# Optimization experiments

Measured on AMD Instinct MI355X. Metric: run time of the kernel, lower is better.

The kernel has to match this reference:

```python
import jax, jax.numpy as jnp
import numpy as np

DIM = 128
N_NODES = 100000
N_EDGES = 1600000


def setup_inputs() -> dict:
    key = jax.random.key(0)
    ks = jax.random.split(key, 9)
    x1 = jax.random.normal(ks[0], (N_NODES, DIM), dtype=jnp.float32)
    x2 = jax.random.normal(ks[1], (N_NODES, DIM), dtype=jnp.float32)
    edge_index = jax.random.randint(ks[2], (2, N_EDGES), 0, N_NODES, dtype=jnp.int64)
    # make_mlp(2*dim, dim, 1, layers=3): Linear(256,128)+ReLU, Linear(128,128)+ReLU, Linear(128,1)
    def lin(k, fan_in, fan_out):
        bound = 1.0 / np.sqrt(fan_in)
        kw, kb = jax.random.split(k)
        W = jax.random.uniform(kw, (fan_in, fan_out), jnp.float32, -bound, bound)
        b = jax.random.uniform(kb, (fan_out,), jnp.float32, -bound, bound)
        return W, b
    W1, b1 = lin(ks[3], 2 * DIM, DIM)
    W2, b2 = lin(ks[4], DIM, DIM)
    W3, b3 = lin(ks[5], DIM, 1)
    return {"x1": x1, "x2": x2, "edge_index": edge_index,
            "W1": W1, "b1": b1, "W2": W2, "b2": b2, "W3": W3, "b3": b3}


def reference(x1, x2, edge_index, W1, b1, W2, b2, W3, b3):
    # Gather endpoints per edge: [E, dim] each
    xs = x1[edge_index[0]]
    xt = x2[edge_index[1]]
    pair = jnp.concatenate([xs, xt], axis=-1)  # [E, 2*dim]
    h = jax.nn.relu(pair @ W1 + b1)            # [E, dim]
    h = jax.nn.relu(h @ W2 + b2)               # [E, dim]
    return h @ W3 + b3                         # [E, 1]
```

## Files before the change

### kernel.cpp

```cpp
#include <hip/hip_runtime.h>
#include <cstdint>

#define DIM 128
#define MTILE 64
#define PAIR_LD 264
#define H_LD 136

typedef __bf16 v8bf __attribute__((ext_vector_type(8)));
typedef float v16f __attribute__((ext_vector_type(16)));

static __device__ __forceinline__ unsigned int f2bf_pack(float a, float b) {
  union { float f; unsigned u; } x, y; x.f = a; y.f = b;
  unsigned lo = (x.u + 0x7FFFu + ((x.u >> 16) & 1u)) >> 16;
  unsigned hi = (y.u + 0x7FFFu + ((y.u >> 16) & 1u)) >> 16;
  return lo | (hi << 16);
}
static __device__ __forceinline__ unsigned short f2bf(float a) {
  union { float f; unsigned u; } x; x.f = a;
  return (unsigned short)((x.u + 0x7FFFu + ((x.u >> 16) & 1u)) >> 16);
}
static __device__ __forceinline__ float bfhi2f(unsigned int hi16) {
  union { unsigned u; float f; } c; c.u = hi16; return c.f;
}

__global__ __launch_bounds__(256) void prep_all(
    const float* __restrict__ W1, const float* __restrict__ W2,
    const float* __restrict__ x1, const float* __restrict__ x2,
    unsigned short* __restrict__ W1t, unsigned short* __restrict__ W2t,
    unsigned short* __restrict__ xc1, unsigned short* __restrict__ xc2,
    int n8, int use_cache) {
  int i = blockIdx.x * 256 + threadIdx.x;
  if (i < 32768) {
    int n = i >> 8, k = i & 255;
    W1t[i] = f2bf(W1[k * 128 + n]);
  } else if (i < 49152) {
    int j = i - 32768;
    int n = j >> 7, k = j & 127;
    W2t[j] = f2bf(W2[k * 128 + n]);
  } else if (use_cache) {
    int j = i - 49152;
    const float* xs;
    unsigned short* xd;
    if (j < n8) { xs = x1; xd = xc1; }
    else if (j < 2 * n8) { xs = x2; xd = xc2; j -= n8; }
    else return;
    const float4* s = reinterpret_cast<const float4*>(xs) + (size_t)j * 2;
    float4 f0 = s[0];
    float4 f1 = s[1];
    uint4 pk;
    pk.x = f2bf_pack(f0.x, f0.y);
    pk.y = f2bf_pack(f0.z, f0.w);
    pk.z = f2bf_pack(f1.x, f1.y);
    pk.w = f2bf_pack(f1.z, f1.w);
    reinterpret_cast<uint4*>(xd)[j] = pk;
  }
}

__global__ __launch_bounds__(256, 2) void mlp_edge_cached(
    const int* __restrict__ eidx,
    const unsigned short* __restrict__ W1t, const unsigned short* __restrict__ W2t,
    const float* __restrict__ b1, const float* __restrict__ b2,
    const float* __restrict__ W3, const float* __restrict__ b3,
    float* __restrict__ out, int E, int ntiles,
    const unsigned short* __restrict__ xc1, const unsigned short* __restrict__ xc2)
{
  __shared__ unsigned short sm_pair[MTILE * PAIR_LD];
  __shared__ unsigned short sm_h1[MTILE * H_LD];
  __shared__ float sm_part[4 * MTILE];

  const int tid = threadIdx.x;
  const int lane = tid & 63;
  const int wv = tid >> 6;
  const int l31 = lane & 31;
  const int l5 = lane >> 5;
  const int nb = wv * 32 + l31;

  v8bf B1[16], B2[8];
#pragma unroll
  for (int kt = 0; kt < 16; ++kt)
    B1[kt] = *reinterpret_cast<const v8bf*>(W1t + nb * 256 + kt * 16 + l5 * 8);
#pragma unroll
  for (int kt = 0; kt < 8; ++kt)
    B2[kt] = *reinterpret_cast<const v8bf*>(W2t + nb * 128 + kt * 16 + l5 * 8);
  const float b1v = b1[nb];
  const float bias3 = b3[0];

  float w3r[16], b2r[16];
#pragma unroll
  for (int r = 0; r < 16; ++r) {
    int n2 = wv * 32 + (r & 3) + 8 * (r >> 2) + 4 * l5;
    w3r[r] = W3[n2];
    b2r[r] = b2[n2];
  }

  const int rslot = tid >> 4;
  const int lane16 = tid & 15;

  int idxr[8];
  {
    const int t0 = min((int)blockIdx.x, ntiles - 1);
    const size_t e0 = (size_t)t0 * MTILE;
#pragma unroll
    for (int p = 0; p < 8; ++p) {
      int el = (p & 3) * 16 + rslot;
      idxr[p] = eidx[e0 + el + ((p >= 4) ? (size_t)E : 0)];
    }
  }

  int eprev = -1;

  for (int tile = blockIdx.x; tile < ntiles; tile += gridDim.x) {
    __syncthreads();

    uint4 xv[8];
#pragma unroll
    for (int p = 0; p < 8; ++p) {
      const unsigned short* xb = (p >= 4) ? xc2 : xc1;
      xv[p] = *reinterpret_cast<const uint4*>(xb + (size_t)idxr[p] * DIM + lane16 * 8);
    }

    if (eprev >= 0 && tid < MTILE) {
      float s = sm_part[tid] + sm_part[64 + tid] + sm_part[128 + tid] + sm_part[192 + tid];
      out[eprev + tid] = s + bias3;
    }

#pragma unroll
    for (int p = 0; p < 8; ++p) {
      int el = (p & 3) * 16 + rslot;
      *reinterpret_cast<uint4*>(&sm_pair[el * PAIR_LD + ((p >= 4) ? 128 : 0) + lane16 * 8]) = xv[p];
    }

    {
      const int tn = min(tile + (int)gridDim.x, ntiles - 1);
      const size_t en = (size_t)tn * MTILE;
#pragma unroll
      for (int p = 0; p < 8; ++p) {
        int el = (p & 3) * 16 + rslot;
        idxr[p] = eidx[en + el + ((p >= 4) ? (size_t)E : 0)];
      }
    }
    __syncthreads();

#pragma unroll
    for (int h = 0; h < 2; ++h) {
      v16f acc;
#pragma unroll
      for (int r = 0; r < 16; ++r) acc[r] = 0.f;
#pragma unroll
      for (int kt = 0; kt < 16; ++kt) {
        v8bf a = *reinterpret_cast<const v8bf*>(&sm_pair[(32 * h + l31) * PAIR_LD + kt * 16 + l5 * 8]);
        acc = __builtin_amdgcn_mfma_f32_32x32x16_bf16(a, B1[kt], acc, 0, 0, 0);
      }
#pragma unroll
      for (int r = 0; r < 16; ++r) {
        int m = 32 * h + (r & 3) + 8 * (r >> 2) + 4 * l5;
        sm_h1[m * H_LD + nb] = f2bf(fmaxf(acc[r] + b1v, 0.f));
      }
    }
    __syncthreads();

#pragma unroll
    for (int h = 0; h < 2; ++h) {
      v16f acc;
#pragma unroll
      for (int r = 0; r < 16; ++r) acc[r] = b2r[r];
#pragma unroll
      for (int kt = 0; kt < 8; ++kt) {
        v8bf bf = *reinterpret_cast<const v8bf*>(&sm_h1[(32 * h + l31) * H_LD + kt * 16 + l5 * 8]);
        acc = __builtin_amdgcn_mfma_f32_32x32x16_bf16(B2[kt], bf, acc, 0, 0, 0);
      }
      float p = 0.f;
#pragma unroll
      for (int r = 0; r < 16; ++r) p += fmaxf(acc[r], 0.f) * w3r[r];
      p += __shfl_xor(p, 32);
      if (l5 == 0) sm_part[wv * 64 + 32 * h + l31] = p;
    }

    eprev = tile * MTILE;
  }

  __syncthreads();
  if (eprev >= 0 && tid < MTILE) {
    float s = sm_part[tid] + sm_part[64 + tid] + sm_part[128 + tid] + sm_part[192 + tid];
    out[eprev + tid] = s + bias3;
  }
}

__global__ __launch_bounds__(256, 2) void mlp_edge_direct(
    const float* __restrict__ x1, const float* __restrict__ x2,
    const int* __restrict__ eidx,
    const unsigned short* __restrict__ W1t, const unsigned short* __restrict__ W2t,
    const float* __restrict__ b1, const float* __restrict__ b2,
    const float* __restrict__ W3, const float* __restrict__ b3,
    float* __restrict__ out, int E, int ntiles)
{
  __shared__ unsigned short sm_pair[MTILE * PAIR_LD];
  __shared__ unsigned short sm_h1[MTILE * H_LD];
  __shared__ float sm_w3[4 * 36];
  unsigned short* sm_h2 = sm_pair;

  const int tid = threadIdx.x;
  const int lane = tid & 63;
  const int wv = tid >> 6;
  const int l31 = lane & 31;
  const int l5 = lane >> 5;
  const int nb = wv * 32 + l31;

  v8bf B1[16], B2[8];
#pragma unroll
  for (int kt = 0; kt < 16; ++kt)
    B1[kt] = *reinterpret_cast<const v8bf*>(W1t + nb * 256 + kt * 16 + l5 * 8);
#pragma unroll
  for (int kt = 0; kt < 8; ++kt)
    B2[kt] = *reinterpret_cast<const v8bf*>(W2t + nb * 128 + kt * 16 + l5 * 8);
  const float b1v = b1[nb];
  const float b2v = b2[nb];
  const float bias3 = b3[0];
  if (tid < 128) sm_w3[(tid >> 5) * 36 + (tid & 31)] = W3[tid];

  const int rslot = tid >> 4;
  const int lane16 = tid & 15;
  const int part = tid & 3;

  for (int tile = blockIdx.x; tile < ntiles; tile += gridDim.x) {
    __syncthreads();
    const int e0 = tile * MTILE;
#pragma unroll
    for (int p = 0; p < 8; ++p) {
      int rowid = p * 16 + rslot;
      int half = rowid >> 6;
      int el = rowid & 63;
      int node = eidx[e0 + el + (half ? E : 0)];
      const float* src = (half ? x2 : x1) + (size_t)node * DIM + lane16 * 8;
      float4 f0 = *reinterpret_cast<const float4*>(src);
      float4 f1 = *reinterpret_cast<const float4*>(src + 4);
      uint4 pk;
      pk.x = f2bf_pack(f0.x, f0.y);
      pk.y = f2bf_pack(f0.z, f0.w);
      pk.z = f2bf_pack(f1.x, f1.y);
      pk.w = f2bf_pack(f1.z, f1.w);
      *reinterpret_cast<uint4*>(&sm_pair[el * PAIR_LD + half * 128 + lane16 * 8]) = pk;
    }
    __syncthreads();

    v16f acc0, acc1;
#pragma unroll
    for (int r = 0; r < 16; ++r) { acc0[r] = 0.f; acc1[r] = 0.f; }
#pragma unroll
    for (int kt = 0; kt < 16; ++kt) {
      v8bf a0 = *reinterpret_cast<const v8bf*>(&sm_pair[l31 * PAIR_LD + kt * 16 + l5 * 8]);
      v8bf a1 = *reinterpret_cast<const v8bf*>(&sm_pair[(32 + l31) * PAIR_LD + kt * 16 + l5 * 8]);
      acc0 = __builtin_amdgcn_mfma_f32_32x32x16_bf16(a0, B1[kt], acc0, 0, 0, 0);
      acc1 = __builtin_amdgcn_mfma_f32_32x32x16_bf16(a1, B1[kt], acc1, 0, 0, 0);
    }
#pragma unroll
    for (int r = 0; r < 16; ++r) {
      int m = (r & 3) + 8 * (r >> 2) + 4 * l5;
      sm_h1[m * H_LD + nb] = f2bf(fmaxf(acc0[r] + b1v, 0.f));
      sm_h1[(32 + m) * H_LD + nb] = f2bf(fmaxf(acc1[r] + b1v, 0.f));
    }
    __syncthreads();

    v16f c0, c1;
#pragma unroll
    for (int r = 0; r < 16; ++r) { c0[r] = 0.f; c1[r] = 0.f; }
#pragma unroll
    for (int kt = 0; kt < 8; ++kt) {
      v8bf a0 = *reinterpret_cast<const v8bf*>(&sm_h1[l31 * H_LD + kt * 16 + l5 * 8]);
      v8bf a1 = *reinterpret_cast<const v8bf*>(&sm_h1[(32 + l31) * H_LD + kt * 16 + l5 * 8]);
      c0 = __builtin_amdgcn_mfma_f32_32x32x16_bf16(a0, B2[kt], c0, 0, 0, 0);
      c1 = __builtin_amdgcn_mfma_f32_32x32x16_bf16(a1, B2[kt], c1, 0, 0, 0);
    }
#pragma unroll
    for (int r = 0; r < 16; ++r) {
      int m = (r & 3) + 8 * (r >> 2) + 4 * l5;
      sm_h2[m * H_LD + nb] = f2bf(fmaxf(c0[r] + b2v, 0.f));
      sm_h2[(32 + m) * H_LD + nb] = f2bf(fmaxf(c1[r] + b2v, 0.f));
    }
    __syncthreads();

    {
      int el = tid >> 2;
      const unsigned short* hrow = &sm_h2[el * H_LD + part * 32];
      const float* wrow = &sm_w3[part * 36];
      float sum = 0.f;
#pragma unroll
      for (int j = 0; j < 4; ++j) {
        uint4 u = *reinterpret_cast<const uint4*>(hrow + j * 8);
        float4 wa = *reinterpret_cast<const float4*>(wrow + j * 8);
        float4 wb = *reinterpret_cast<const float4*>(wrow + j * 8 + 4);
        sum += bfhi2f(u.x << 16) * wa.x + bfhi2f(u.x & 0xFFFF0000u) * wa.y;
        sum += bfhi2f(u.y << 16) * wa.z + bfhi2f(u.y & 0xFFFF0000u) * wa.w;
        sum += bfhi2f(u.z << 16) * wb.x + bfhi2f(u.z & 0xFFFF0000u) * wb.y;
        sum += bfhi2f(u.w << 16) * wb.z + bfhi2f(u.w & 0xFFFF0000u) * wb.w;
      }
      sum += __shfl_xor(sum, 1, 64);
      sum += __shfl_xor(sum, 2, 64);
      if (part == 0) out[e0 + el] = sum + bias3;
    }
  }
}

extern "C" void kernel_launch(void* const* d_in, const int* in_sizes, int n_in,
                              void* d_out, int out_size, void* d_ws, size_t ws_size,
                              hipStream_t stream) {
  const float* x1 = (const float*)d_in[0];
  const float* x2 = (const float*)d_in[1];
  const int* eidx = (const int*)d_in[2];
  const float* W1 = (const float*)d_in[3];
  const float* b1 = (const float*)d_in[4];
  const float* W2 = (const float*)d_in[5];
  const float* b2 = (const float*)d_in[6];
  const float* W3 = (const float*)d_in[7];
  const float* b3 = (const float*)d_in[8];
  float* out = (float*)d_out;

  int E = in_sizes[2] / 2;
  if (E <= 0) return;
  int ntiles = E / MTILE;
  int nelem = in_sizes[0];
  int n8 = nelem / 8;

  unsigned short* W1t = (unsigned short*)d_ws;
  unsigned short* W2t = W1t + 32768;
  size_t woff = 98304;
  size_t need = woff + 2 * (size_t)nelem * 2;
  int use_cache = (ws_size >= need) ? 1 : 0;
  unsigned short* xc1 = (unsigned short*)((char*)d_ws + woff);
  unsigned short* xc2 = xc1 + nelem;

  int prep_items = 49152 + (use_cache ? 2 * n8 : 0);
  prep_all<<<(prep_items + 255) / 256, 256, 0, stream>>>(
      W1, W2, x1, x2, W1t, W2t, xc1, xc2, n8, use_cache);

  if (use_cache) {
    mlp_edge_cached<<<512, 256, 0, stream>>>(eidx, W1t, W2t, b1, b2, W3, b3,
                                             out, E, ntiles, xc1, xc2);
  } else {
    mlp_edge_direct<<<512, 256, 0, stream>>>(x1, x2, eidx, W1t, W2t,
                                             b1, b2, W3, b3, out, E, ntiles);
  }
}
```

Baseline: 315.6 us.

## Precompute first-layer projections per node and gather projected features per edge

Because the first linear layer is linear in the concatenated inputs, x1@W1a and x2@W1b+b1 are computed once per node in a new kernel and stored as fp16. The edge kernel then gathers the two projected rows, adds them, applies ReLU and runs only the second GEMM, using fp16 MFMA. This cuts first-layer MFMA work from per edge (1.6M) to per node (200k) and drops the pair shared-memory buffer, which allows higher occupancy and a larger grid. The cost is an extra launch and fp16 rounding of the layer-one outputs, which differs slightly from bf16 numerics.

```diff
diff --git a/kernel.cpp b/kernel.cpp
--- a/kernel.cpp
+++ b/kernel.cpp
@@ -7,6 +7,7 @@
 #define H_LD 136
 
 typedef __bf16 v8bf __attribute__((ext_vector_type(8)));
+typedef _Float16 v8hf __attribute__((ext_vector_type(8)));
 typedef float v16f __attribute__((ext_vector_type(16)));
 
 static __device__ __forceinline__ unsigned int f2bf_pack(float a, float b) {
@@ -19,16 +20,17 @@
   union { float f; unsigned u; } x; x.f = a;
   return (unsigned short)((x.u + 0x7FFFu + ((x.u >> 16) & 1u)) >> 16);
 }
+static __device__ __forceinline__ unsigned short f2h(float a) {
+  union { _Float16 h; unsigned short u; } c; c.h = (_Float16)a; return c.u;
+}
 static __device__ __forceinline__ float bfhi2f(unsigned int hi16) {
   union { unsigned u; float f; } c; c.u = hi16; return c.f;
 }
 
-__global__ __launch_bounds__(256) void prep_all(
+__global__ __launch_bounds__(256) void prep_w(
     const float* __restrict__ W1, const float* __restrict__ W2,
-    const float* __restrict__ x1, const float* __restrict__ x2,
     unsigned short* __restrict__ W1t, unsigned short* __restrict__ W2t,
-    unsigned short* __restrict__ xc1, unsigned short* __restrict__ xc2,
-    int n8, int use_cache) {
+    int w2_f16) {
   int i = blockIdx.x * 256 + threadIdx.x;
   if (i < 32768) {
     int n = i >> 8, k = i & 255;
@@ -36,37 +38,19 @@
   } else if (i < 49152) {
     int j = i - 32768;
     int n = j >> 7, k = j & 127;
-    W2t[j] = f2bf(W2[k * 128 + n]);
-  } else if (use_cache) {
-    int j = i - 49152;
-    const float* xs;
-    unsigned short* xd;
-    if (j < n8) { xs = x1; xd = xc1; }
-    else if (j < 2 * n8) { xs = x2; xd = xc2; j -= n8; }
-    else return;
-    const float4* s = reinterpret_cast<const float4*>(xs) + (size_t)j * 2;
-    float4 f0 = s[0];
-    float4 f1 = s[1];
-    uint4 pk;
-    pk.x = f2bf_pack(f0.x, f0.y);
-    pk.y = f2bf_pack(f0.z, f0.w);
-    pk.z = f2bf_pack(f1.x, f1.y);
-    pk.w = f2bf_pack(f1.z, f1.w);
-    reinterpret_cast<uint4*>(xd)[j] = pk;
-  }
-}
-
-__global__ __launch_bounds__(256, 2) void mlp_edge_cached(
-    const int* __restrict__ eidx,
-    const unsigned short* __restrict__ W1t, const unsigned short* __restrict__ W2t,
-    const float* __restrict__ b1, const float* __restrict__ b2,
-    const float* __restrict__ W3, const float* __restrict__ b3,
-    float* __restrict__ out, int E, int ntiles,
-    const unsigned short* __restrict__ xc1, const unsigned short* __restrict__ xc2)
+    float v = W2[k * 128 + n];
+    W2t[j] = w2_f16 ? f2h(v) : f2bf(v);
+  }
+}
+
+__global__ __launch_bounds__(256, 2) void node_precompute(
+    const float* __restrict__ x1, const float* __restrict__ x2,
+    const unsigned short* __restrict__ W1t, const float* __restrict__ b1,
+    unsigned short* __restrict__ y1c, unsigned short* __restrict__ y2c,
+    int nnodes)
 {
-  __shared__ unsigned short sm_pair[MTILE * PAIR_LD];
-  __shared__ unsigned short sm_h1[MTILE * H_LD];
-  __shared__ float sm_part[4 * MTILE];
+  __shared__ unsigned short sm_x[MTILE * H_LD];
+  __shared__ unsigned short sm_y[MTILE * H_LD];
 
   const int tid = threadIdx.x;
   const int lane = tid & 63;
@@ -74,15 +58,89 @@
   const int l31 = lane & 31;
   const int l5 = lane >> 5;
   const int nb = wv * 32 + l31;
-
-  v8bf B1[16], B2[8];
+  const int rslot = tid >> 4;
+  const int lane16 = tid & 15;
+  const int base = blockIdx.x * MTILE;
+  const int nvalid = nnodes - base;
+
+  v8bf B1[16];
 #pragma unroll
   for (int kt = 0; kt < 16; ++kt)
     B1[kt] = *reinterpret_cast<const v8bf*>(W1t + nb * 256 + kt * 16 + l5 * 8);
+  const float b1v = b1[nb];
+
+#pragma unroll 1
+  for (int which = 0; which < 2; ++which) {
+    const float* xs = which ? x2 : x1;
+#pragma unroll
+    for (int p = 0; p < 4; ++p) {
+      int el = p * 16 + rslot;
+      int row = base + el; if (row >= nnodes) row = nnodes - 1;
+      const float4* s = reinterpret_cast<const float4*>(xs + (size_t)row * DIM) + lane16 * 2;
+      float4 f0 = s[0];
+      float4 f1 = s[1];
+      uint4 pk;
+      pk.x = f2bf_pack(f0.x, f0.y);
+      pk.y = f2bf_pack(f0.z, f0.w);
+      pk.z = f2bf_pack(f1.x, f1.y);
+      pk.w = f2bf_pack(f1.z, f1.w);
+      *reinterpret_cast<uint4*>(&sm_x[el * H_LD + lane16 * 8]) = pk;
+    }
+    __syncthreads();
+
+#pragma unroll
+    for (int h = 0; h < 2; ++h) {
+      v16f acc;
+#pragma unroll
+      for (int r = 0; r < 16; ++r) acc[r] = 0.f;
+#pragma unroll
+      for (int kt = 0; kt < 8; ++kt) {
+        v8bf a = *reinterpret_cast<const v8bf*>(&sm_x[(32 * h + l31) * H_LD + kt * 16 + l5 * 8]);
+        acc = __builtin_amdgcn_mfma_f32_32x32x16_bf16(a, B1[which * 8 + kt], acc, 0, 0, 0);
+      }
+#pragma unroll
+      for (int r = 0; r < 16; ++r) {
+        int m = 32 * h + (r & 3) + 8 * (r >> 2) + 4 * l5;
+        float v = acc[r] + (which ? b1v : 0.f);
+        sm_y[m * H_LD + nb] = f2h(v);
+      }
+    }
+    __syncthreads();
+
+    unsigned short* yd = which ? y2c : y1c;
+#pragma unroll
+    for (int p = 0; p < 4; ++p) {
+      int el = p * 16 + rslot;
+      if (el < nvalid)
+        *reinterpret_cast<uint4*>(yd + (size_t)(base + el) * DIM + lane16 * 8) =
+            *reinterpret_cast<const uint4*>(&sm_y[el * H_LD + lane16 * 8]);
+    }
+    __syncthreads();
+  }
+}
+
+__global__ __launch_bounds__(256, 4) void mlp_edge_y(
+    const int* __restrict__ eidx,
+    const unsigned short* __restrict__ W2t,
+    const float* __restrict__ b2, const float* __restrict__ W3,
+    const float* __restrict__ b3, float* __restrict__ out,
+    int E, int ntiles,
+    const unsigned short* __restrict__ y1c, const unsigned short* __restrict__ y2c)
+{
+  __shared__ unsigned short sm_h1[MTILE * H_LD];
+  __shared__ float sm_part[4 * MTILE];
+
+  const int tid = threadIdx.x;
+  const int lane = tid & 63;
+  const int wv = tid >> 6;
+  const int l31 = lane & 31;
+  const int l5 = lane >> 5;
+  const int nb = wv * 32 + l31;
+
+  v8hf B2[8];
 #pragma unroll
   for (int kt = 0; kt < 8; ++kt)
-    B2[kt] = *reinterpret_cast<const v8bf*>(W2t + nb * 128 + kt * 16 + l5 * 8);
-  const float b1v = b1[nb];
+    B2[kt] = *reinterpret_cast<const v8hf*>(W2t + nb * 128 + kt * 16 + l5 * 8);
   const float bias3 = b3[0];
 
   float w3r[16], b2r[16];
@@ -112,11 +170,11 @@
   for (int tile = blockIdx.x; tile < ntiles; tile += gridDim.x) {
     __syncthreads();
 
-    uint4 xv[8];
-#pragma unroll
-    for (int p = 0; p < 8; ++p) {
-      const unsigned short* xb = (p >= 4) ? xc2 : xc1;
-      xv[p] = *reinterpret_cast<const uint4*>(xb + (size_t)idxr[p] * DIM + lane16 * 8);
+    uint4 av[4], bv[4];
+#pragma unroll
+    for (int p = 0; p < 4; ++p) {
+      av[p] = *reinterpret_cast<const uint4*>(y1c + (size_t)idxr[p] * DIM + lane16 * 8);
+      bv[p] = *reinterpret_cast<const uint4*>(y2c + (size_t)idxr[p + 4] * DIM + lane16 * 8);
     }
 
     if (eprev >= 0 && tid < MTILE) {
@@ -125,9 +183,15 @@
     }
 
 #pragma unroll
-    for (int p = 0; p < 8; ++p) {
-      int el = (p & 3) * 16 + rslot;
-      *reinterpret_cast<uint4*>(&sm_pair[el * PAIR_LD + ((p >= 4) ? 128 : 0) + lane16 * 8]) = xv[p];
+    for (int p = 0; p < 4; ++p) {
+      union { uint4 u; v8hf h; } a, b;
+      a.u = av[p]; b.u = bv[p];
+      v8hf s = a.h + b.h;
+#pragma unroll
+      for (int j = 0; j < 8; ++j) s[j] = s[j] > (_Float16)0 ? s[j] : (_Float16)0;
+      union { v8hf h; uint4 u; } r; r.h = s;
+      int el = p * 16 + rslot;
+      *reinterpret_cast<uint4*>(&sm_h1[el * H_LD + lane16 * 8]) = r.u;
     }
 
     {
@@ -145,29 +209,11 @@
     for (int h = 0; h < 2; ++h) {
       v16f acc;
 #pragma unroll
-      for (int r = 0; r < 16; ++r) acc[r] = 0.f;
-#pragma unroll
-      for (int kt = 0; kt < 16; ++kt) {
-        v8bf a = *reinterpret_cast<const v8bf*>(&sm_pair[(32 * h + l31) * PAIR_LD + kt * 16 + l5 * 8]);
-        acc = __builtin_amdgcn_mfma_f32_32x32x16_bf16(a, B1[kt], acc, 0, 0, 0);
-      }
-#pragma unroll
-      for (int r = 0; r < 16; ++r) {
-        int m = 32 * h + (r & 3) + 8 * (r >> 2) + 4 * l5;
-        sm_h1[m * H_LD + nb] = f2bf(fmaxf(acc[r] + b1v, 0.f));
-      }
-    }
-    __syncthreads();
-
-#pragma unroll
-    for (int h = 0; h < 2; ++h) {
-      v16f acc;
-#pragma unroll
       for (int r = 0; r < 16; ++r) acc[r] = b2r[r];
 #pragma unroll
       for (int kt = 0; kt < 8; ++kt) {
-        v8bf bf = *reinterpret_cast<const v8bf*>(&sm_h1[(32 * h + l31) * H_LD + kt * 16 + l5 * 8]);
-        acc = __builtin_amdgcn_mfma_f32_32x32x16_bf16(B2[kt], bf, acc, 0, 0, 0);
+        v8hf bf = *reinterpret_cast<const v8hf*>(&sm_h1[(32 * h + l31) * H_LD + kt * 16 + l5 * 8]);
+        acc = __builtin_amdgcn_mfma_f32_32x32x16_f16(B2[kt], bf, acc, 0, 0, 0);
       }
       float p = 0.f;
 #pragma unroll
@@ -319,23 +365,23 @@
   if (E <= 0) return;
   int ntiles = E / MTILE;
   int nelem = in_sizes[0];
-  int n8 = nelem / 8;
+  int nnodes = nelem / DIM;
 
   unsigned short* W1t = (unsigned short*)d_ws;
   unsigned short* W2t = W1t + 32768;
   size_t woff = 98304;
   size_t need = woff + 2 * (size_t)nelem * 2;
   int use_cache = (ws_size >= need) ? 1 : 0;
-  unsigned short* xc1 = (unsigned short*)((char*)d_ws + woff);
-  unsigned short* xc2 = xc1 + nelem;
-
-  int prep_items = 49152 + (use_cache ? 2 * n8 : 0);
-  prep_all<<<(prep_items + 255) / 256, 256, 0, stream>>>(
-      W1, W2, x1, x2, W1t, W2t, xc1, xc2, n8, use_cache);
+  unsigned short* y1c = (unsigned short*)((char*)d_ws + woff);
+  unsigned short* y2c = y1c + nelem;
+
+  prep_w<<<192, 256, 0, stream>>>(W1, W2, W1t, W2t, use_cache);
 
   if (use_cache) {
-    mlp_edge_cached<<<512, 256, 0, stream>>>(eidx, W1t, W2t, b1, b2, W3, b3,
-                                             out, E, ntiles, xc1, xc2);
+    node_precompute<<<(nnodes + MTILE - 1) / MTILE, 256, 0, stream>>>(
+        x1, x2, W1t, b1, y1c, y2c, nnodes);
+    mlp_edge_y<<<1024, 256, 0, stream>>>(eidx, W2t, b2, W3, b3,
+                                         out, E, ntiles, y1c, y2c);
   } else {
     mlp_edge_direct<<<512, 256, 0, stream>>>(x1, x2, eidx, W1t, W2t,
                                              b1, b2, W3, b3, out, E, ntiles);
```

Result: faster. 296.6 us (-6.0%).
